# Optimization experiments

Hardware: AMD Instinct MI355X
Metric: run time of the kernel (lower is better)

The kernel has to match this reference:

```python
import jax, jax.numpy as jnp
import numpy as np

B, T, N, D = 4, 4, 256, 128  # batch, time_steps, num_nodes, features (in==out)
EPS = 1e-5
NEG = -1e9


def _glorot(key, shape):
    fan_in, fan_out = shape[0], shape[1]
    s = float(np.sqrt(6.0 / (fan_in + fan_out)))
    return jax.random.uniform(key, shape, jnp.float32, -s, s)


def setup_inputs() -> dict:
    key = jax.random.key(0)
    ks = jax.random.split(key, 8)
    x = jax.random.normal(ks[0], (B, T, N, D), jnp.float32)
    adj = (jax.random.uniform(ks[1], (N, N)) < 0.05).astype(jnp.float32)
    adj = jnp.maximum(adj, jnp.eye(N, dtype=jnp.float32))
    weight = _glorot(ks[2], (D, D))            # GCN weight [in, out]
    bias = jnp.zeros((D,), jnp.float32)
    att_w1 = _glorot(ks[3], (2 * D, D))        # Linear(2D -> D), column layout
    att_b1 = jnp.zeros((D,), jnp.float32)
    att_w2 = _glorot(ks[4], (D, 1))            # Linear(D -> 1)
    att_b2 = jnp.zeros((1,), jnp.float32)
    ln_gamma = jnp.ones((D,), jnp.float32)
    ln_beta = jnp.zeros((D,), jnp.float32)
    return dict(x=x, adj_matrix=adj, weight=weight, bias=bias,
                att_w1=att_w1, att_b1=att_b1, att_w2=att_w2, att_b2=att_b2,
                ln_gamma=ln_gamma, ln_beta=ln_beta)


def _layer_norm(y, gamma, beta):
    mu = jnp.mean(y, axis=-1, keepdims=True)
    var = jnp.mean(jnp.square(y - mu), axis=-1, keepdims=True)
    return (y - mu) * jax.lax.rsqrt(var + EPS) * gamma + beta


def reference(x, adj_matrix, weight, bias, att_w1, att_b1, att_w2, att_b2,
              ln_gamma, ln_beta):
    d_out = weight.shape[1]
    # split the first attention Linear so cat([h_i, h_j]) @ W1 == h_i@W1a + h_j@W1b
    W1a, W1b = att_w1[:d_out], att_w1[d_out:]
    w2 = att_w2[:, 0]
    mask = adj_matrix[None] == 0  # [1, N, N]

    def step(carry, x_t):  # x_t: [B, N, D]
        h = x_t @ weight + bias                                  # [B, N, D]
        a = h @ W1a                                              # [B, N, D]
        b = h @ W1b                                              # [B, N, D]
        # big intermediate the kernel would fuse away: [B, N, N, D]
        e = jax.nn.leaky_relu(a[:, :, None, :] + b[:, None, :, :] + att_b1, 0.2)
        scores = jnp.einsum('bijd,d->bij', e, w2) + att_b2[0]    # [B, N, N]
        scores = jnp.where(mask, NEG, scores)
        attn = jax.nn.softmax(scores, axis=-1)  # dropout is identity in eval
        agg = jnp.einsum('bij,bjd->bid', attn, h)                # [B, N, D]
        out = _layer_norm(agg + x_t, ln_gamma, ln_beta)          # in==out residual
        return carry, out

    _, ys = jax.lax.scan(step, None, jnp.swapaxes(x, 0, 1))      # [T, B, N, D]
    return jax.nn.relu(jnp.swapaxes(ys, 0, 1))                   # [B, T, N, D]
```

## Files before the change

kernel.cpp:

```cpp
#include <hip/hip_runtime.h>
#include <hip/hip_bf16.h>

#define BT 16
#define NN 256
#define DD 128
#define MROWS (BT*NN)

typedef __bf16 bf16x8 __attribute__((ext_vector_type(8)));
typedef __bf16 bf16x2 __attribute__((ext_vector_type(2)));
typedef float  f32x4  __attribute__((ext_vector_type(4)));

#define LREL(z) ((z) >= 0.0f ? (z) : 0.2f * (z))
#define HS_STRIDE 136

__global__ __launch_bounds__(256) void gemm2_kernel(
        const float* __restrict__ x, const float* __restrict__ weight,
        const float* __restrict__ bias, const float* __restrict__ attw1,
        const float* __restrict__ attb1,
        __bf16* __restrict__ hbuf, __bf16* __restrict__ abuf,
        __bf16* __restrict__ bbuf) {
    int tid = threadIdx.x;
    int w = tid >> 6, l = tid & 63;
    int chunk = blockIdx.x >> 1, parity = blockIdx.x & 1;
    int row0 = chunk * 16;
    int lrow = l & 15, lk8 = (l >> 4) * 8;

    __shared__ __align__(16) __bf16 hs[16][HS_STRIDE];

    const float* abase = x + (size_t)(row0 + lrow) * DD + lk8;
    bf16x8 af[4];
#pragma unroll
    for (int kt = 0; kt < 4; ++kt) {
        float4 u0 = *(const float4*)(abase + 32 * kt);
        float4 u1 = *(const float4*)(abase + 32 * kt + 4);
        af[kt][0]=(__bf16)u0.x; af[kt][1]=(__bf16)u0.y;
        af[kt][2]=(__bf16)u0.z; af[kt][3]=(__bf16)u0.w;
        af[kt][4]=(__bf16)u1.x; af[kt][5]=(__bf16)u1.y;
        af[kt][6]=(__bf16)u1.z; af[kt][7]=(__bf16)u1.w;
    }

#pragma unroll
    for (int s = 0; s < 2; ++s) {
        int n0 = (w + 4 * s) * 16;
        int ncol = n0 + lrow;
        bf16x8 wf[4];
#pragma unroll
        for (int kt = 0; kt < 4; ++kt) {
            const float* wp = weight + (size_t)(lk8 + 32 * kt) * DD + ncol;
#pragma unroll
            for (int j = 0; j < 8; ++j)
                wf[kt][j] = (__bf16)wp[(size_t)j * DD];
        }
        f32x4 acc = {0.f, 0.f, 0.f, 0.f};
        acc = __builtin_amdgcn_mfma_f32_16x16x32_bf16(af[0], wf[0], acc, 0, 0, 0);
        acc = __builtin_amdgcn_mfma_f32_16x16x32_bf16(af[1], wf[1], acc, 0, 0, 0);
        acc = __builtin_amdgcn_mfma_f32_16x16x32_bf16(af[2], wf[2], acc, 0, 0, 0);
        acc = __builtin_amdgcn_mfma_f32_16x16x32_bf16(af[3], wf[3], acc, 0, 0, 0);

        float bb = bias[ncol];
        int rloc = (l >> 4) * 4;
        __bf16* hout = hbuf + (size_t)(row0 + rloc) * DD + ncol;
#pragma unroll
        for (int r = 0; r < 4; ++r) {
            __bf16 hv = (__bf16)(acc[r] + bb);
            hs[rloc + r][ncol] = hv;
            if (parity == 0) hout[(size_t)r * DD] = hv;
        }
    }
    __syncthreads();

    bf16x8 ha[4];
#pragma unroll
    for (int kt = 0; kt < 4; ++kt)
        ha[kt] = *(const bf16x8*)(&hs[lrow][lk8 + 32 * kt]);

#pragma unroll
    for (int s = 0; s < 2; ++s) {
        int n0 = (w + 4 * s) * 16;
        int ncol = n0 + lrow;
        bf16x8 w1f[4];
#pragma unroll
        for (int kt = 0; kt < 4; ++kt) {
            const float* wp = attw1 + (size_t)(parity * DD + lk8 + 32 * kt) * DD + ncol;
#pragma unroll
            for (int j = 0; j < 8; ++j)
                w1f[kt][j] = (__bf16)wp[(size_t)j * DD];
        }
        f32x4 acc = {0.f, 0.f, 0.f, 0.f};
        acc = __builtin_amdgcn_mfma_f32_16x16x32_bf16(ha[0], w1f[0], acc, 0, 0, 0);
        acc = __builtin_amdgcn_mfma_f32_16x16x32_bf16(ha[1], w1f[1], acc, 0, 0, 0);
        acc = __builtin_amdgcn_mfma_f32_16x16x32_bf16(ha[2], w1f[2], acc, 0, 0, 0);
        acc = __builtin_amdgcn_mfma_f32_16x16x32_bf16(ha[3], w1f[3], acc, 0, 0, 0);

        float bb = parity ? attb1[ncol] : 0.f;
        __bf16* dst = (parity ? bbuf : abuf) + (size_t)(row0 + (l >> 4) * 4) * DD + ncol;
#pragma unroll
        for (int r = 0; r < 4; ++r)
            dst[(size_t)r * DD] = (__bf16)(acc[r] + bb);
    }
}

__global__ __launch_bounds__(256) void attn_kernel(
        const __bf16* __restrict__ hbuf, const __bf16* __restrict__ abuf,
        const __bf16* __restrict__ bbuf, const float* __restrict__ x,
        const float* __restrict__ adj, const float* __restrict__ w2,
        const float* __restrict__ gamma, const float* __restrict__ beta,
        float* __restrict__ out) {
    int tid = threadIdx.x;
    int w = tid >> 6, l = tid & 63;
    int i  = (blockIdx.x & 63) * 4 + w;
    int bt = blockIdx.x >> 6;
    int d2 = 2 * l;

    __shared__ int nbr_l[4][64];

    int cnt = 0;
    const float* adjrow = adj + (size_t)i * NN;
    for (int jt = 0; jt < NN / 64; ++jt) {
        int j = jt * 64 + l;
        float v = adjrow[j];
        unsigned long long mask = __ballot(v != 0.f);
        if (v != 0.f) {
            int pos = cnt + __popcll(mask & ((1ull << l) - 1ull));
            if (pos < 64) nbr_l[w][pos] = j;
        }
        cnt += __popcll(mask);
    }
    cnt = min(cnt, 64);
    int jreg = nbr_l[w][l];

    bf16x2 av = *(const bf16x2*)(abuf + (size_t)(bt * NN + i) * DD + d2);
    float a0 = (float)av[0], a1 = (float)av[1];
    float2 wv = *(const float2*)(w2 + d2);
    float w20 = wv.x, w21 = wv.y;
    const __bf16* bbase = bbuf + (size_t)bt * NN * DD;

    float m = -3.0e38f, myp = 0.f;
    int c = 0;
    for (; c + 3 < cnt; c += 4) {
        int j0 = __shfl(jreg, c),     j1 = __shfl(jreg, c + 1);
        int j2 = __shfl(jreg, c + 2), j3 = __shfl(jreg, c + 3);
        bf16x2 b0 = *(const bf16x2*)(bbase + (size_t)j0 * DD + d2);
        bf16x2 b1 = *(const bf16x2*)(bbase + (size_t)j1 * DD + d2);
        bf16x2 b2 = *(const bf16x2*)(bbase + (size_t)j2 * DD + d2);
        bf16x2 b3 = *(const bf16x2*)(bbase + (size_t)j3 * DD + d2);
        float p0 = LREL(a0 + (float)b0[0]) * w20 + LREL(a1 + (float)b0[1]) * w21;
        float p1 = LREL(a0 + (float)b1[0]) * w20 + LREL(a1 + (float)b1[1]) * w21;
        float p2 = LREL(a0 + (float)b2[0]) * w20 + LREL(a1 + (float)b2[1]) * w21;
        float p3 = LREL(a0 + (float)b3[0]) * w20 + LREL(a1 + (float)b3[1]) * w21;
#pragma unroll
        for (int off = 32; off; off >>= 1) {
            p0 += __shfl_xor(p0, off);
            p1 += __shfl_xor(p1, off);
            p2 += __shfl_xor(p2, off);
            p3 += __shfl_xor(p3, off);
        }
        myp = (l == c)     ? p0 : myp;
        myp = (l == c + 1) ? p1 : myp;
        myp = (l == c + 2) ? p2 : myp;
        myp = (l == c + 3) ? p3 : myp;
        m = fmaxf(m, fmaxf(fmaxf(p0, p1), fmaxf(p2, p3)));
    }
    for (; c < cnt; ++c) {
        int j0 = __shfl(jreg, c);
        bf16x2 b0 = *(const bf16x2*)(bbase + (size_t)j0 * DD + d2);
        float p0 = LREL(a0 + (float)b0[0]) * w20 + LREL(a1 + (float)b0[1]) * w21;
#pragma unroll
        for (int off = 32; off; off >>= 1) p0 += __shfl_xor(p0, off);
        myp = (l == c) ? p0 : myp;
        m = fmaxf(m, p0);
    }

    float wgt = (l < cnt) ? __expf(myp - m) : 0.f;
    float dsum = wgt;
#pragma unroll
    for (int off = 32; off; off >>= 1) dsum += __shfl_xor(dsum, off);
    float inv = 1.f / dsum;

    const __bf16* hbase = hbuf + (size_t)bt * NN * DD;
    float acc0 = 0.f, acc1 = 0.f;
    c = 0;
    for (; c + 3 < cnt; c += 4) {
        float wc0 = __shfl(wgt, c),     wc1 = __shfl(wgt, c + 1);
        float wc2 = __shfl(wgt, c + 2), wc3 = __shfl(wgt, c + 3);
        int j0 = __shfl(jreg, c),     j1 = __shfl(jreg, c + 1);
        int j2 = __shfl(jreg, c + 2), j3 = __shfl(jreg, c + 3);
        bf16x2 h0 = *(const bf16x2*)(hbase + (size_t)j0 * DD + d2);
        bf16x2 h1 = *(const bf16x2*)(hbase + (size_t)j1 * DD + d2);
        bf16x2 h2 = *(const bf16x2*)(hbase + (size_t)j2 * DD + d2);
        bf16x2 h3 = *(const bf16x2*)(hbase + (size_t)j3 * DD + d2);
        acc0 += wc0 * (float)h0[0] + wc1 * (float)h1[0]
              + wc2 * (float)h2[0] + wc3 * (float)h3[0];
        acc1 += wc0 * (float)h0[1] + wc1 * (float)h1[1]
              + wc2 * (float)h2[1] + wc3 * (float)h3[1];
    }
    for (; c < cnt; ++c) {
        float wc = __shfl(wgt, c);
        int j = __shfl(jreg, c);
        bf16x2 h0 = *(const bf16x2*)(hbase + (size_t)j * DD + d2);
        acc0 += wc * (float)h0[0];
        acc1 += wc * (float)h0[1];
    }

    float2 xv = *(const float2*)(x + (size_t)(bt * NN + i) * DD + d2);
    float y0 = acc0 * inv + xv.x;
    float y1 = acc1 * inv + xv.y;

    float s = y0 + y1;
#pragma unroll
    for (int off = 32; off; off >>= 1) s += __shfl_xor(s, off);
    float mu = s * (1.0f / 128.0f);
    float v0 = y0 - mu, v1 = y1 - mu;
    float vs = v0 * v0 + v1 * v1;
#pragma unroll
    for (int off = 32; off; off >>= 1) vs += __shfl_xor(vs, off);
    float rstd = rsqrtf(vs * (1.0f / 128.0f) + 1e-5f);

    float2 gv = *(const float2*)(gamma + d2);
    float2 bv = *(const float2*)(beta + d2);
    float2 ov;
    ov.x = fmaxf(v0 * rstd * gv.x + bv.x, 0.0f);
    ov.y = fmaxf(v1 * rstd * gv.y + bv.y, 0.0f);
    *(float2*)(out + (size_t)(bt * NN + i) * DD + d2) = ov;
}

extern "C" void kernel_launch(void* const* d_in, const int* in_sizes, int n_in,
                              void* d_out, int out_size, void* d_ws, size_t ws_size,
                              hipStream_t stream) {
    const float* x      = (const float*)d_in[0];
    const float* adj    = (const float*)d_in[1];
    const float* weight = (const float*)d_in[2];
    const float* bias   = (const float*)d_in[3];
    const float* attw1  = (const float*)d_in[4];
    const float* attb1  = (const float*)d_in[5];
    const float* attw2  = (const float*)d_in[6];
    const float* gamma  = (const float*)d_in[8];
    const float* beta   = (const float*)d_in[9];
    float* out = (float*)d_out;

    char* p = (char*)d_ws;
    __bf16* hbuf = (__bf16*)p;        p += (size_t)MROWS * DD * 2;
    __bf16* abuf = (__bf16*)p;        p += (size_t)MROWS * DD * 2;
    __bf16* bbuf = (__bf16*)p;

    gemm2_kernel<<<MROWS / 16 * 2, 256, 0, stream>>>(x, weight, bias, attw1, attb1,
                                                     hbuf, abuf, bbuf);
    attn_kernel<<<NN / 4 * BT, 256, 0, stream>>>(hbuf, abuf, bbuf, x, adj,
                                                 attw2, gamma, beta, out);
}
```

Before: 26.95 us.

## Precompute neighbor lists in GEMM kernel and fuse online softmax with aggregation

The adjacency-row compaction into neighbor lists moves out of the attention kernel, where it was repeated for every batch-time slice, into the first GEMM kernel, which computes it once per node and writes it to workspace. The attention kernel now runs a single pass with an online softmax: it loads the b and h rows together and rescales the running sum and accumulators each step, instead of doing a score pass and then a separate weighted-sum pass. This removes redundant adjacency reads and a second gather loop. In exchange it adds extra exp and rescale work per group of four neighbors, makes the tail padding always load the node's own rows, and depends on the ordering between the two kernels.

```diff
diff --git a/kernel.cpp b/kernel.cpp
--- a/kernel.cpp
+++ b/kernel.cpp
@@ -16,9 +16,10 @@
 __global__ __launch_bounds__(256) void gemm2_kernel(
         const float* __restrict__ x, const float* __restrict__ weight,
         const float* __restrict__ bias, const float* __restrict__ attw1,
-        const float* __restrict__ attb1,
+        const float* __restrict__ attb1, const float* __restrict__ adj,
         __bf16* __restrict__ hbuf, __bf16* __restrict__ abuf,
-        __bf16* __restrict__ bbuf) {
+        __bf16* __restrict__ bbuf, int* __restrict__ nbr,
+        int* __restrict__ nbr_cnt) {
     int tid = threadIdx.x;
     int w = tid >> 6, l = tid & 63;
     int chunk = blockIdx.x >> 1, parity = blockIdx.x & 1;
@@ -26,6 +27,23 @@
     int lrow = l & 15, lk8 = (l >> 4) * 8;
 
     __shared__ __align__(16) __bf16 hs[16][HS_STRIDE];
+
+    if (parity == 0 && w == 0) {
+        int i = chunk;
+        int cnt = 0;
+        const float* adjrow = adj + (size_t)i * NN;
+        for (int jt = 0; jt < NN / 64; ++jt) {
+            int j = jt * 64 + l;
+            float v = adjrow[j];
+            unsigned long long mask = __ballot(v != 0.f);
+            if (v != 0.f) {
+                int pos = cnt + __popcll(mask & ((1ull << l) - 1ull));
+                if (pos < 64) nbr[i * 64 + pos] = j;
+            }
+            cnt += __popcll(mask);
+        }
+        if (l == 0) nbr_cnt[i] = min(cnt, 64);
+    }
 
     const float* abase = x + (size_t)(row0 + lrow) * DD + lk8;
     bf16x8 af[4];
@@ -103,47 +121,42 @@
 __global__ __launch_bounds__(256) void attn_kernel(
         const __bf16* __restrict__ hbuf, const __bf16* __restrict__ abuf,
         const __bf16* __restrict__ bbuf, const float* __restrict__ x,
-        const float* __restrict__ adj, const float* __restrict__ w2,
-        const float* __restrict__ gamma, const float* __restrict__ beta,
-        float* __restrict__ out) {
+        const int* __restrict__ nbr, const int* __restrict__ nbr_cnt,
+        const float* __restrict__ w2, const float* __restrict__ gamma,
+        const float* __restrict__ beta, float* __restrict__ out) {
     int tid = threadIdx.x;
     int w = tid >> 6, l = tid & 63;
     int i  = (blockIdx.x & 63) * 4 + w;
     int bt = blockIdx.x >> 6;
     int d2 = 2 * l;
 
-    __shared__ int nbr_l[4][64];
-
-    int cnt = 0;
-    const float* adjrow = adj + (size_t)i * NN;
-    for (int jt = 0; jt < NN / 64; ++jt) {
-        int j = jt * 64 + l;
-        float v = adjrow[j];
-        unsigned long long mask = __ballot(v != 0.f);
-        if (v != 0.f) {
-            int pos = cnt + __popcll(mask & ((1ull << l) - 1ull));
-            if (pos < 64) nbr_l[w][pos] = j;
-        }
-        cnt += __popcll(mask);
-    }
-    cnt = min(cnt, 64);
-    int jreg = nbr_l[w][l];
+    int cnt = nbr_cnt[i];
+    int jreg = nbr[i * 64 + l];
 
     bf16x2 av = *(const bf16x2*)(abuf + (size_t)(bt * NN + i) * DD + d2);
     float a0 = (float)av[0], a1 = (float)av[1];
     float2 wv = *(const float2*)(w2 + d2);
     float w20 = wv.x, w21 = wv.y;
     const __bf16* bbase = bbuf + (size_t)bt * NN * DD;
-
-    float m = -3.0e38f, myp = 0.f;
-    int c = 0;
-    for (; c + 3 < cnt; c += 4) {
-        int j0 = __shfl(jreg, c),     j1 = __shfl(jreg, c + 1);
-        int j2 = __shfl(jreg, c + 2), j3 = __shfl(jreg, c + 3);
+    const __bf16* hbase = hbuf + (size_t)bt * NN * DD;
+
+    float m = -3.0e38f, dsum = 0.f, acc0 = 0.f, acc1 = 0.f;
+    for (int c = 0; c < cnt; c += 4) {
+        int i0 = c, i1 = c + 1, i2 = c + 2, i3 = c + 3;
+        bool v1 = i1 < cnt, v2 = i2 < cnt, v3 = i3 < cnt;
+        int j0 = __shfl(jreg, i0);
+        int j1 = v1 ? __shfl(jreg, i1) : i;
+        int j2 = v2 ? __shfl(jreg, i2) : i;
+        int j3 = v3 ? __shfl(jreg, i3) : i;
         bf16x2 b0 = *(const bf16x2*)(bbase + (size_t)j0 * DD + d2);
         bf16x2 b1 = *(const bf16x2*)(bbase + (size_t)j1 * DD + d2);
         bf16x2 b2 = *(const bf16x2*)(bbase + (size_t)j2 * DD + d2);
         bf16x2 b3 = *(const bf16x2*)(bbase + (size_t)j3 * DD + d2);
+        bf16x2 h0 = *(const bf16x2*)(hbase + (size_t)j0 * DD + d2);
+        bf16x2 h1 = *(const bf16x2*)(hbase + (size_t)j1 * DD + d2);
+        bf16x2 h2 = *(const bf16x2*)(hbase + (size_t)j2 * DD + d2);
+        bf16x2 h3 = *(const bf16x2*)(hbase + (size_t)j3 * DD + d2);
+
         float p0 = LREL(a0 + (float)b0[0]) * w20 + LREL(a1 + (float)b0[1]) * w21;
         float p1 = LREL(a0 + (float)b1[0]) * w20 + LREL(a1 + (float)b1[1]) * w21;
         float p2 = LREL(a0 + (float)b2[0]) * w20 + LREL(a1 + (float)b2[1]) * w21;
@@ -155,52 +168,24 @@
             p2 += __shfl_xor(p2, off);
             p3 += __shfl_xor(p3, off);
         }
-        myp = (l == c)     ? p0 : myp;
-        myp = (l == c + 1) ? p1 : myp;
-        myp = (l == c + 2) ? p2 : myp;
-        myp = (l == c + 3) ? p3 : myp;
-        m = fmaxf(m, fmaxf(fmaxf(p0, p1), fmaxf(p2, p3)));
-    }
-    for (; c < cnt; ++c) {
-        int j0 = __shfl(jreg, c);
-        bf16x2 b0 = *(const bf16x2*)(bbase + (size_t)j0 * DD + d2);
-        float p0 = LREL(a0 + (float)b0[0]) * w20 + LREL(a1 + (float)b0[1]) * w21;
-#pragma unroll
-        for (int off = 32; off; off >>= 1) p0 += __shfl_xor(p0, off);
-        myp = (l == c) ? p0 : myp;
-        m = fmaxf(m, p0);
-    }
-
-    float wgt = (l < cnt) ? __expf(myp - m) : 0.f;
-    float dsum = wgt;
-#pragma unroll
-    for (int off = 32; off; off >>= 1) dsum += __shfl_xor(dsum, off);
+        float pm0 = p0;
+        float pm1 = v1 ? p1 : -3.0e38f;
+        float pm2 = v2 ? p2 : -3.0e38f;
+        float pm3 = v3 ? p3 : -3.0e38f;
+        float m_new = fmaxf(m, fmaxf(fmaxf(pm0, pm1), fmaxf(pm2, pm3)));
+        float scale = __expf(m - m_new);
+        float e0 = __expf(p0 - m_new);
+        float e1 = v1 ? __expf(p1 - m_new) : 0.f;
+        float e2 = v2 ? __expf(p2 - m_new) : 0.f;
+        float e3 = v3 ? __expf(p3 - m_new) : 0.f;
+        dsum = dsum * scale + (e0 + e1) + (e2 + e3);
+        acc0 = acc0 * scale + e0 * (float)h0[0] + e1 * (float)h1[0]
+                            + e2 * (float)h2[0] + e3 * (float)h3[0];
+        acc1 = acc1 * scale + e0 * (float)h0[1] + e1 * (float)h1[1]
+                            + e2 * (float)h2[1] + e3 * (float)h3[1];
+        m = m_new;
+    }
     float inv = 1.f / dsum;
-
-    const __bf16* hbase = hbuf + (size_t)bt * NN * DD;
-    float acc0 = 0.f, acc1 = 0.f;
-    c = 0;
-    for (; c + 3 < cnt; c += 4) {
-        float wc0 = __shfl(wgt, c),     wc1 = __shfl(wgt, c + 1);
-        float wc2 = __shfl(wgt, c + 2), wc3 = __shfl(wgt, c + 3);
-        int j0 = __shfl(jreg, c),     j1 = __shfl(jreg, c + 1);
-        int j2 = __shfl(jreg, c + 2), j3 = __shfl(jreg, c + 3);
-        bf16x2 h0 = *(const bf16x2*)(hbase + (size_t)j0 * DD + d2);
-        bf16x2 h1 = *(const bf16x2*)(hbase + (size_t)j1 * DD + d2);
-        bf16x2 h2 = *(const bf16x2*)(hbase + (size_t)j2 * DD + d2);
-        bf16x2 h3 = *(const bf16x2*)(hbase + (size_t)j3 * DD + d2);
-        acc0 += wc0 * (float)h0[0] + wc1 * (float)h1[0]
-              + wc2 * (float)h2[0] + wc3 * (float)h3[0];
-        acc1 += wc0 * (float)h0[1] + wc1 * (float)h1[1]
-              + wc2 * (float)h2[1] + wc3 * (float)h3[1];
-    }
-    for (; c < cnt; ++c) {
-        float wc = __shfl(wgt, c);
-        int j = __shfl(jreg, c);
-        bf16x2 h0 = *(const bf16x2*)(hbase + (size_t)j * DD + d2);
-        acc0 += wc * (float)h0[0];
-        acc1 += wc * (float)h0[1];
-    }
 
     float2 xv = *(const float2*)(x + (size_t)(bt * NN + i) * DD + d2);
     float y0 = acc0 * inv + xv.x;
@@ -241,10 +226,13 @@
     char* p = (char*)d_ws;
     __bf16* hbuf = (__bf16*)p;        p += (size_t)MROWS * DD * 2;
     __bf16* abuf = (__bf16*)p;        p += (size_t)MROWS * DD * 2;
-    __bf16* bbuf = (__bf16*)p;
+    __bf16* bbuf = (__bf16*)p;        p += (size_t)MROWS * DD * 2;
+    int* nbr     = (int*)p;           p += (size_t)NN * 64 * 4;
+    int* nbr_cnt = (int*)p;
 
     gemm2_kernel<<<MROWS / 16 * 2, 256, 0, stream>>>(x, weight, bias, attw1, attb1,
-                                                     hbuf, abuf, bbuf);
-    attn_kernel<<<NN / 4 * BT, 256, 0, stream>>>(hbuf, abuf, bbuf, x, adj,
+                                                     adj, hbuf, abuf, bbuf,
+                                                     nbr, nbr_cnt);
+    attn_kernel<<<NN / 4 * BT, 256, 0, stream>>>(hbuf, abuf, bbuf, x, nbr, nbr_cnt,
                                                  attw2, gamma, beta, out);
 }
```

Result: faster. 24.02 us (median of 2 runs) (-10.9%).
